# Kernel optimization log

Hardware: AMD Instinct MI355X
Metric: run time of the kernel (lower is better)

Reference implementation:

```python
import jax, jax.numpy as jnp
import numpy as np

N_NODES = 100_000
N_EDGES = 1_600_000
HID = 64
TXT = 384
N_LAYERS = 2
BATCH = 1024


def setup_inputs() -> dict:
    key = jax.random.key(0)
    ks = jax.random.split(key, 13)
    s = 0.05
    return {
        "text_emb": jax.random.normal(ks[0], (N_NODES, TXT), dtype=jnp.float32),
        "weights": jax.random.uniform(ks[1], (N_EDGES,), dtype=jnp.float32),
        "W_enc": jax.random.normal(ks[2], (TXT, HID), dtype=jnp.float32) * s,
        "b_enc": jax.random.normal(ks[3], (HID,), dtype=jnp.float32) * s,
        "Wself_f": jax.random.normal(ks[4], (N_LAYERS, HID, HID), dtype=jnp.float32) * s,
        "Wneigh_f": jax.random.normal(ks[5], (N_LAYERS, HID, HID), dtype=jnp.float32) * s,
        "b_f": jax.random.normal(ks[6], (N_LAYERS, HID), dtype=jnp.float32) * s,
        "Wself_r": jax.random.normal(ks[7], (N_LAYERS, HID, HID), dtype=jnp.float32) * s,
        "Wneigh_r": jax.random.normal(ks[8], (N_LAYERS, HID, HID), dtype=jnp.float32) * s,
        "b_r": jax.random.normal(ks[9], (N_LAYERS, HID), dtype=jnp.float32) * s,
        "src": jax.random.randint(ks[10], (N_EDGES,), 0, N_NODES, dtype=jnp.int32),
        "dst": jax.random.randint(ks[11], (N_EDGES,), 0, N_NODES, dtype=jnp.int32),
        "ids_idx": jax.random.randint(ks[12], (BATCH,), 0, N_NODES, dtype=jnp.int32),
    }


def _inv_degree(idx, n, e_dtype):
    deg = jax.ops.segment_sum(jnp.ones((idx.shape[0],), dtype=e_dtype), idx, num_segments=n)
    return jnp.where(deg > 0, 1.0 / deg, 0.0)  # zero in-degree -> 0 (DGL mean)


def _sage_mean(x, src, dst, w, inv_deg, Wself, Wneigh, b):
    # DGL SAGEConv('mean') with edge_weight: neigh = mean_over_in_edges(w * h_src)
    m = w[:, None] * x[src]                                   # [E, H] gather
    neigh = jax.ops.segment_sum(m, dst, num_segments=x.shape[0]) * inv_deg[:, None]
    return x @ Wself + neigh @ Wneigh + b


def reference(text_emb, weights, W_enc, b_enc, Wself_f, Wneigh_f, b_f,
              Wself_r, Wneigh_r, b_r, src, dst, ids_idx):
    n = text_emb.shape[0]
    inv_f = _inv_degree(dst, n, text_emb.dtype)   # forward graph: aggregate into dst
    inv_r = _inv_degree(src, n, text_emb.dtype)   # reversed graph: aggregate into src
    x = text_emb @ W_enc + b_enc                  # text encoder
    for l in range(Wself_f.shape[0]):
        y = jax.nn.relu(_sage_mean(x, src, dst, weights, inv_f,
                                   Wself_f[l], Wneigh_f[l], b_f[l]))
        y = y + jax.nn.relu(_sage_mean(x, dst, src, weights, inv_r,
                                       Wself_r[l], Wneigh_r[l], b_r[l]))
        x = x + y                                 # skip connection
    feat = x[ids_idx]                             # [B, H]
    return feat / jnp.linalg.norm(feat, axis=1, keepdims=True)
```

## Files before the change

### kernel.cpp

```cpp
#include <hip/hip_runtime.h>

#define NN 100000
#define NE 1600000
#define HID 64
#define TXT 384
#define BATCH 1024
#define NBUCK 391
#define SBLK 256
#define EPB ((NE + SBLK - 1) / SBLK)
#define LDA 40
#define LDK2 72

typedef __attribute__((ext_vector_type(8))) short short8;
typedef __attribute__((ext_vector_type(4))) float float4v;

__device__ __forceinline__ ushort f2bf(float f) {
  unsigned u = __float_as_uint(f);
  unsigned r = (u + 0x7fffu + ((u >> 16) & 1u)) >> 16;
  return (ushort)r;
}
__device__ __forceinline__ float bf2f(ushort u) {
  return __uint_as_float(((unsigned)u) << 16);
}
__device__ __forceinline__ short8 pack8(float4 a, float4 b) {
  short8 s;
  s[0] = (short)f2bf(a.x); s[1] = (short)f2bf(a.y);
  s[2] = (short)f2bf(a.z); s[3] = (short)f2bf(a.w);
  s[4] = (short)f2bf(b.x); s[5] = (short)f2bf(b.y);
  s[6] = (short)f2bf(b.z); s[7] = (short)f2bf(b.w);
  return s;
}

__global__ void k_clear(unsigned char* __restrict__ idmap,
                        unsigned char* __restrict__ flag, int* __restrict__ nf) {
  int i = blockIdx.x * 256 + threadIdx.x;
  if (i < NN) { idmap[i] = 0; flag[i] = 0; }
  if (i == 0) *nf = 0;
}

__global__ void k_seed(const int* __restrict__ ids,
                       unsigned char* __restrict__ idmap,
                       unsigned char* __restrict__ flag) {
  int b = blockIdx.x * 256 + threadIdx.x;
  if (b < BATCH) { int r = ids[b]; idmap[r] = 1; flag[r] = 1; }
}

__global__ void k_fedges(const int* __restrict__ src, const int* __restrict__ dst,
                         const unsigned char* __restrict__ idmap,
                         unsigned char* __restrict__ flag) {
  const int t = threadIdx.x, blk = blockIdx.x;
  const int e0 = blk * EPB, e1 = min(NE, e0 + EPB);
  for (int e = e0 + t; e < e1; e += 256) {
    int s = src[e], d = dst[e];
    if (idmap[d]) flag[s] = 1;
    if (idmap[s]) flag[d] = 1;
  }
}

__global__ void k_compact(const unsigned char* __restrict__ flag,
                          int* __restrict__ frows, int* __restrict__ nf) {
  int i = blockIdx.x * 256 + threadIdx.x;
  if (i < NN && flag[i]) frows[atomicAdd(nf, 1)] = i;
}

__global__ void k_hist2(const int* __restrict__ src, const int* __restrict__ dst,
                        const unsigned char* __restrict__ flag,
                        int* __restrict__ cm_f, int* __restrict__ cm_r) {
  __shared__ int hf[NBUCK], hr[NBUCK];
  const int t = threadIdx.x, blk = blockIdx.x;
  for (int i = t; i < NBUCK; i += 256) { hf[i] = 0; hr[i] = 0; }
  __syncthreads();
  const int e0 = blk * EPB, e1 = min(NE, e0 + EPB);
  for (int e = e0 + t; e < e1; e += 256) {
    int s = src[e], d = dst[e];
    if (flag[d]) atomicAdd(&hf[d >> 8], 1);
    if (flag[s]) atomicAdd(&hr[s >> 8], 1);
  }
  __syncthreads();
  for (int i = t; i < NBUCK; i += 256) {
    cm_f[i * SBLK + blk] = hf[i];
    cm_r[i * SBLK + blk] = hr[i];
  }
}

__global__ void k_scan1(int* __restrict__ cm_f, int* __restrict__ cm_r,
                        int* __restrict__ btot) {
  __shared__ int tmp[256];
  const int t = threadIdx.x;
  int b = blockIdx.x;
  int* cm = (b < NBUCK) ? cm_f : cm_r;
  int bucket = (b < NBUCK) ? b : b - NBUCK;
  int* row = cm + bucket * SBLK;
  int v = row[t];
  tmp[t] = v; __syncthreads();
  for (int d = 1; d < 256; d <<= 1) {
    int s = tmp[t]; if (t >= d) s += tmp[t - d];
    __syncthreads(); tmp[t] = s; __syncthreads();
  }
  row[t] = tmp[t] - v;
  if (t == 255) btot[b] = tmp[t];
}

__global__ void k_scan2(const int* __restrict__ btot,
                        int* __restrict__ bbase_f, int* __restrict__ bbase_r) {
  __shared__ int tmp[512];
  const int t = threadIdx.x;
  int h = (t < NBUCK) ? btot[t] : 0;
  tmp[t] = h; __syncthreads();
  for (int d = 1; d < 512; d <<= 1) {
    int v = tmp[t]; if (t >= d) v += tmp[t - d];
    __syncthreads(); tmp[t] = v; __syncthreads();
  }
  if (t < NBUCK) bbase_f[t] = tmp[t] - h;
  __syncthreads();
  h = (t < NBUCK) ? btot[NBUCK + t] : 0;
  tmp[t] = h; __syncthreads();
  for (int d = 1; d < 512; d <<= 1) {
    int v = tmp[t]; if (t >= d) v += tmp[t - d];
    __syncthreads(); tmp[t] = v; __syncthreads();
  }
  if (t < NBUCK) bbase_r[t] = tmp[t] - h;
}

__global__ void k_scatter2(const int* __restrict__ src, const int* __restrict__ dst,
                           const float* __restrict__ w,
                           const unsigned char* __restrict__ flag,
                           const int* __restrict__ cm_f, const int* __restrict__ cm_r,
                           const int* __restrict__ bbase_f, const int* __restrict__ bbase_r,
                           int2* __restrict__ stg_f, int2* __restrict__ stg_r) {
  __shared__ int cur_f[NBUCK], cur_r[NBUCK];
  const int t = threadIdx.x, blk = blockIdx.x;
  for (int i = t; i < NBUCK; i += 256) {
    cur_f[i] = bbase_f[i] + cm_f[i * SBLK + blk];
    cur_r[i] = bbase_r[i] + cm_r[i * SBLK + blk];
  }
  __syncthreads();
  const int e0 = blk * EPB, e1 = min(NE, e0 + EPB);
  for (int e = e0 + t; e < e1; e += 256) {
    int s = src[e], d = dst[e];
    int wb = __float_as_int(w[e]);
    if (flag[d]) {
      int p = atomicAdd(&cur_f[d >> 8], 1);
      stg_f[p] = make_int2(((d & 255) << 24) | s, wb);
    }
    if (flag[s]) {
      int q = atomicAdd(&cur_r[s >> 8], 1);
      stg_r[q] = make_int2(((s & 255) << 24) | d, wb);
    }
  }
}

__global__ void p_build(const unsigned char* __restrict__ flag,
                        const int2* __restrict__ stgf, const int* __restrict__ btotf,
                        const int* __restrict__ bbasef,
                        int* __restrict__ startf, int* __restrict__ cntf,
                        int2* __restrict__ cvf, int* __restrict__ permf,
                        const int2* __restrict__ stgr, const int* __restrict__ btotr,
                        const int* __restrict__ bbaser,
                        int* __restrict__ startr, int* __restrict__ cntr,
                        int2* __restrict__ cvr, int* __restrict__ permr) {
  int b = blockIdx.x;
  const int2* stg; const int* bcnt; const int* bbase;
  int* start; int* cnt; int2* cv; int* perm;
  if (b < NBUCK) { stg = stgf; bcnt = btotf; bbase = bbasef; start = startf; cnt = cntf; cv = cvf; perm = permf; }
  else { b -= NBUCK; stg = stgr; bcnt = btotr; bbase = bbaser; start = startr; cnt = cntr; cv = cvr; perm = permr; }
  const int base = bbase[b];
  const int n = bcnt[b];
  const int t = threadIdx.x;
  __shared__ int hist[256], tmp[256], cur[256], dh[256], dc[256];
  hist[t] = 0;
  perm[b * 256 + t] = -1;
  __syncthreads();
  for (int i = t; i < n; i += 256) {
    unsigned pk = (unsigned)stg[base + i].x;
    atomicAdd(&hist[pk >> 24], 1);
  }
  __syncthreads();
  const int h = hist[t];
  tmp[t] = h; __syncthreads();
  for (int d = 1; d < 256; d <<= 1) {
    int v = tmp[t]; if (t >= d) v += tmp[t - d];
    __syncthreads(); tmp[t] = v; __syncthreads();
  }
  const int excl = tmp[t] - h;
  const int node = (b << 8) + t;
  const bool valid = (node < NN) && flag[node];
  if (valid) { start[node] = base + excl; cnt[node] = h; }
  cur[t] = excl;
  dh[t] = 0; __syncthreads();
  const int dcap = min(h, 255);
  if (valid) atomicAdd(&dh[dcap], 1);
  __syncthreads();
  int dv = dh[t];
  tmp[t] = dv; __syncthreads();
  for (int d = 1; d < 256; d <<= 1) {
    int v = tmp[t]; if (t >= d) v += tmp[t - d];
    __syncthreads(); tmp[t] = v; __syncthreads();
  }
  dc[t] = tmp[t] - dv;
  __syncthreads();
  if (valid) {
    int pos = atomicAdd(&dc[dcap], 1);
    perm[b * 256 + pos] = node;
  }
  __syncthreads();
  for (int i = t; i < n; i += 256) {
    int2 en = stg[base + i];
    unsigned d8 = ((unsigned)en.x) >> 24;
    int pos = atomicAdd(&cur[d8], 1);
    cv[base + pos] = make_int2(en.x & 0xFFFFFF, en.y);
  }
}

__global__ void k_gather3(const ushort* __restrict__ xb,
                          const int* __restrict__ permf, const int* __restrict__ startf,
                          const int* __restrict__ cntf, const int2* __restrict__ cvf,
                          ushort* __restrict__ nbf,
                          const int* __restrict__ permr, const int* __restrict__ startr,
                          const int* __restrict__ cntr, const int2* __restrict__ cvr,
                          ushort* __restrict__ nbr) {
  const int BPD = (NBUCK * 256) / 16;
  int b = blockIdx.x;
  const int *perm, *start, *cnt; const int2* cv; ushort* outp;
  if (b < BPD) { perm = permf; start = startf; cnt = cntf; cv = cvf; outp = nbf; }
  else { b -= BPD; perm = permr; start = startr; cnt = cntr; cv = cvr; outp = nbr; }
  const int lane = threadIdx.x & 63;
  const int wave = threadIdx.x >> 6;
  const int slot = b * 16 + wave * 4 + (lane >> 4);
  const int fl = (lane & 15) * 4;
  const int row = perm[slot];
  if (row < 0) return;
  const int s = start[row], c = cnt[row];
  const int e = s + c;
  float a0 = 0.f, a1 = 0.f, a2 = 0.f, a3 = 0.f;
  int j = s;
  for (; j + 4 <= e; j += 4) {
    int2 e0 = cv[j], e1 = cv[j + 1], e2 = cv[j + 2], e3 = cv[j + 3];
    uint2 v0 = *(const uint2*)(xb + (size_t)e0.x * 64 + fl);
    uint2 v1 = *(const uint2*)(xb + (size_t)e1.x * 64 + fl);
    uint2 v2 = *(const uint2*)(xb + (size_t)e2.x * 64 + fl);
    uint2 v3 = *(const uint2*)(xb + (size_t)e3.x * 64 + fl);
    float w0 = __int_as_float(e0.y), w1 = __int_as_float(e1.y);
    float w2 = __int_as_float(e2.y), w3 = __int_as_float(e3.y);
    a0 += w0 * bf2f((ushort)v0.x); a1 += w0 * bf2f((ushort)(v0.x >> 16));
    a2 += w0 * bf2f((ushort)v0.y); a3 += w0 * bf2f((ushort)(v0.y >> 16));
    a0 += w1 * bf2f((ushort)v1.x); a1 += w1 * bf2f((ushort)(v1.x >> 16));
    a2 += w1 * bf2f((ushort)v1.y); a3 += w1 * bf2f((ushort)(v1.y >> 16));
    a0 += w2 * bf2f((ushort)v2.x); a1 += w2 * bf2f((ushort)(v2.x >> 16));
    a2 += w2 * bf2f((ushort)v2.y); a3 += w2 * bf2f((ushort)(v2.y >> 16));
    a0 += w3 * bf2f((ushort)v3.x); a1 += w3 * bf2f((ushort)(v3.x >> 16));
    a2 += w3 * bf2f((ushort)v3.y); a3 += w3 * bf2f((ushort)(v3.y >> 16));
  }
  for (; j < e; ++j) {
    int2 ee = cv[j];
    uint2 v = *(const uint2*)(xb + (size_t)ee.x * 64 + fl);
    float ww = __int_as_float(ee.y);
    a0 += ww * bf2f((ushort)v.x); a1 += ww * bf2f((ushort)(v.x >> 16));
    a2 += ww * bf2f((ushort)v.y); a3 += ww * bf2f((ushort)(v.y >> 16));
  }
  float inv = (c > 0) ? 1.0f / (float)c : 0.f;
  uint2 pv;
  pv.x = (uint)f2bf(a0 * inv) | ((uint)f2bf(a1 * inv) << 16);
  pv.y = (uint)f2bf(a2 * inv) | ((uint)f2bf(a3 * inv) << 16);
  *(uint2*)(outp + (size_t)row * 64 + fl) = pv;
}

__global__ void k_bgather(const ushort* __restrict__ xb, const int* __restrict__ ids,
                          const int* __restrict__ startf, const int* __restrict__ cntf,
                          const int2* __restrict__ cvf, ushort* __restrict__ nbf,
                          const int* __restrict__ startr, const int* __restrict__ cntr,
                          const int2* __restrict__ cvr, ushort* __restrict__ nbr) {
  const int lane = threadIdx.x & 63;
  const int wave = threadIdx.x >> 6;
  const int fl = (lane & 15) * 4;
  const int t = blockIdx.x * 16 + wave * 4 + (lane >> 4);
  const int rev = (t >= BATCH);
  const int b = rev ? t - BATCH : t;
  const int row = ids[b];
  const int* start = rev ? startr : startf;
  const int* cnt   = rev ? cntr   : cntf;
  const int2* cv   = rev ? cvr    : cvf;
  ushort* outp     = rev ? nbr    : nbf;
  const int s = start[row], c = cnt[row];
  const int e = s + c;
  float a0 = 0.f, a1 = 0.f, a2 = 0.f, a3 = 0.f;
  int j = s;
  for (; j + 4 <= e; j += 4) {
    int2 e0 = cv[j], e1 = cv[j + 1], e2 = cv[j + 2], e3 = cv[j + 3];
    uint2 v0 = *(const uint2*)(xb + (size_t)e0.x * 64 + fl);
    uint2 v1 = *(const uint2*)(xb + (size_t)e1.x * 64 + fl);
    uint2 v2 = *(const uint2*)(xb + (size_t)e2.x * 64 + fl);
    uint2 v3 = *(const uint2*)(xb + (size_t)e3.x * 64 + fl);
    float w0 = __int_as_float(e0.y), w1 = __int_as_float(e1.y);
    float w2 = __int_as_float(e2.y), w3 = __int_as_float(e3.y);
    a0 += w0 * bf2f((ushort)v0.x); a1 += w0 * bf2f((ushort)(v0.x >> 16));
    a2 += w0 * bf2f((ushort)v0.y); a3 += w0 * bf2f((ushort)(v0.y >> 16));
    a0 += w1 * bf2f((ushort)v1.x); a1 += w1 * bf2f((ushort)(v1.x >> 16));
    a2 += w1 * bf2f((ushort)v1.y); a3 += w1 * bf2f((ushort)(v1.y >> 16));
    a0 += w2 * bf2f((ushort)v2.x); a1 += w2 * bf2f((ushort)(v2.x >> 16));
    a2 += w2 * bf2f((ushort)v2.y); a3 += w2 * bf2f((ushort)(v2.y >> 16));
    a0 += w3 * bf2f((ushort)v3.x); a1 += w3 * bf2f((ushort)(v3.x >> 16));
    a2 += w3 * bf2f((ushort)v3.y); a3 += w3 * bf2f((ushort)(v3.y >> 16));
  }
  for (; j < e; ++j) {
    int2 ee = cv[j];
    uint2 v = *(const uint2*)(xb + (size_t)ee.x * 64 + fl);
    float ww = __int_as_float(ee.y);
    a0 += ww * bf2f((ushort)v.x); a1 += ww * bf2f((ushort)(v.x >> 16));
    a2 += ww * bf2f((ushort)v.y); a3 += ww * bf2f((ushort)(v.y >> 16));
  }
  float inv = (c > 0) ? 1.0f / (float)c : 0.f;
  uint2 pv;
  pv.x = (uint)f2bf(a0 * inv) | ((uint)f2bf(a1 * inv) << 16);
  pv.y = (uint)f2bf(a2 * inv) | ((uint)f2bf(a3 * inv) << 16);
  *(uint2*)(outp + (size_t)b * 64 + fl) = pv;
}

__global__ void k_wtile(const float* __restrict__ W, ushort* __restrict__ Wt) {
  int b = blockIdx.x;
  int ch = b >> 2, nt = b & 3;
  int lane = threadIdx.x;
  int quad = lane >> 4, lr = lane & 15;
  short8 s;
  #pragma unroll
  for (int j = 0; j < 8; ++j)
    s[j] = (short)f2bf(W[(ch * 32 + quad * 8 + j) * 64 + nt * 16 + lr]);
  *(short8*)&Wt[((size_t)b * 64 + lane) * 8] = s;
}

__launch_bounds__(256)
__global__ void k_enc3(const float* __restrict__ T, const ushort* __restrict__ Wt,
                       const float* __restrict__ bias,
                       float* __restrict__ x, ushort* __restrict__ xb) {
  __shared__ short As[2][128 * LDA];
  const int tid = threadIdx.x;
  const int row0 = blockIdx.x * 128;
  const int wave = tid >> 6, lane = tid & 63;
  const int quad = lane >> 4, lr = lane & 15;
  const int srow = tid >> 1, shalf = (tid & 1) * 16;
  const int grow = min(row0 + srow, NN - 1);
  const float* tp = T + (size_t)grow * TXT + shalf;

  float4 pa0 = *(const float4*)(tp);
  float4 pa1 = *(const float4*)(tp + 4);
  float4 pa2 = *(const float4*)(tp + 8);
  float4 pa3 = *(const float4*)(tp + 12);
  *(short8*)&As[0][srow * LDA + shalf] = pack8(pa0, pa1);
  *(short8*)&As[0][srow * LDA + shalf + 8] = pack8(pa2, pa3);
  pa0 = *(const float4*)(tp + 32);
  pa1 = *(const float4*)(tp + 36);
  pa2 = *(const float4*)(tp + 40);
  pa3 = *(const float4*)(tp + 44);
  __syncthreads();

  const ushort* pw = Wt + lane * 8;
  float4v acc[2][4] = {};
  #pragma unroll
  for (int ch = 0; ch < 12; ++ch) {
    const short* Ac = As[ch & 1];
    short8 af0 = *(const short8*)&Ac[(wave * 32 + lr) * LDA + quad * 8];
    short8 af1 = *(const short8*)&Ac[(wave * 32 + 16 + lr) * LDA + quad * 8];
    #pragma unroll
    for (int nt = 0; nt < 4; ++nt) {
      short8 bfrag = *(const short8*)(pw + (size_t)(ch * 4 + nt) * 512);
      acc[0][nt] = __builtin_amdgcn_mfma_f32_16x16x32_bf16(af0, bfrag, acc[0][nt], 0, 0, 0);
      acc[1][nt] = __builtin_amdgcn_mfma_f32_16x16x32_bf16(af1, bfrag, acc[1][nt], 0, 0, 0);
    }
    if (ch < 11) {
      short* An = As[(ch + 1) & 1];
      *(short8*)&An[srow * LDA + shalf] = pack8(pa0, pa1);
      *(short8*)&An[srow * LDA + shalf + 8] = pack8(pa2, pa3);
      if (ch + 2 < 12) {
        const float* q = tp + (ch + 2) * 32;
        pa0 = *(const float4*)(q);
        pa1 = *(const float4*)(q + 4);
        pa2 = *(const float4*)(q + 8);
        pa3 = *(const float4*)(q + 12);
      }
      __syncthreads();
    }
  }
  #pragma unroll
  for (int nt = 0; nt < 4; ++nt) {
    const int col = nt * 16 + lr;
    const float bcol = bias[col];
    #pragma unroll
    for (int mt = 0; mt < 2; ++mt) {
      #pragma unroll
      for (int r = 0; r < 4; ++r) {
        const int row = row0 + wave * 32 + mt * 16 + quad * 4 + r;
        if (row < NN) {
          float v = acc[mt][nt][r] + bcol;
          x[(size_t)row * 64 + col] = v;
          xb[(size_t)row * 64 + col] = f2bf(v);
        }
      }
    }
  }
}

__launch_bounds__(256)
__global__ void k_layerf(const int* __restrict__ frows, const int* __restrict__ nfp,
                         const ushort* __restrict__ xbin,
                         const ushort* __restrict__ nbf, const ushort* __restrict__ nbr,
                         const float* __restrict__ Wsf, const float* __restrict__ Wnf,
                         const float* __restrict__ bfv,
                         const float* __restrict__ Wsr, const float* __restrict__ Wnr,
                         const float* __restrict__ brv,
                         float* __restrict__ x, ushort* __restrict__ xb) {
  const int nfv = *nfp;
  const int row0 = blockIdx.x * 128;
  if (row0 >= nfv) return;
  __shared__ short B4[4 * 64 * LDK2];
  __shared__ short As[128 * LDK2];
  const int tid = threadIdx.x;
  const int wave = tid >> 6, lane = tid & 63;
  const int quad = lane >> 4, lr = lane & 15;

  {
    #pragma unroll
    for (int j = 0; j < 16; ++j) {
      int idx = j * 256 + tid;
      int k = idx >> 6, n = idx & 63;
      B4[0 * 64 * LDK2 + n * LDK2 + k] = (short)f2bf(Wsf[idx]);
      B4[1 * 64 * LDK2 + n * LDK2 + k] = (short)f2bf(Wsr[idx]);
      B4[2 * 64 * LDK2 + n * LDK2 + k] = (short)f2bf(Wnf[idx]);
      B4[3 * 64 * LDK2 + n * LDK2 + k] = (short)f2bf(Wnr[idx]);
    }
  }
  const int srow = tid >> 1, half = (tid & 1) * 32;
  const int slot = row0 + srow;
  const int grow = frows[(slot < nfv) ? slot : 0];
  {
    const uint4* s = (const uint4*)(xbin + (size_t)grow * 64 + half);
    uint4* d = (uint4*)&As[srow * LDK2 + half];
    d[0] = s[0]; d[1] = s[1]; d[2] = s[2]; d[3] = s[3];
  }
  const uint4* pf = (const uint4*)(nbf + (size_t)grow * 64 + half);
  uint4 p0 = pf[0], p1 = pf[1], p2 = pf[2], p3 = pf[3];
  __syncthreads();

  float4v accf[2][4] = {}, accr[2][4] = {};
  #pragma unroll
  for (int kk = 0; kk < 64; kk += 32) {
    short8 a0 = *(const short8*)&As[(wave * 32 + lr) * LDK2 + kk + quad * 8];
    short8 a1 = *(const short8*)&As[(wave * 32 + 16 + lr) * LDK2 + kk + quad * 8];
    #pragma unroll
    for (int nt = 0; nt < 4; ++nt) {
      short8 bs = *(const short8*)&B4[0 * 64 * LDK2 + (nt * 16 + lr) * LDK2 + kk + quad * 8];
      accf[0][nt] = __builtin_amdgcn_mfma_f32_16x16x32_bf16(a0, bs, accf[0][nt], 0, 0, 0);
      accf[1][nt] = __builtin_amdgcn_mfma_f32_16x16x32_bf16(a1, bs, accf[1][nt], 0, 0, 0);
      short8 bq = *(const short8*)&B4[1 * 64 * LDK2 + (nt * 16 + lr) * LDK2 + kk + quad * 8];
      accr[0][nt] = __builtin_amdgcn_mfma_f32_16x16x32_bf16(a0, bq, accr[0][nt], 0, 0, 0);
      accr[1][nt] = __builtin_amdgcn_mfma_f32_16x16x32_bf16(a1, bq, accr[1][nt], 0, 0, 0);
    }
  }
  __syncthreads();
  { uint4* d = (uint4*)&As[srow * LDK2 + half]; d[0] = p0; d[1] = p1; d[2] = p2; d[3] = p3; }
  {
    const uint4* pr = (const uint4*)(nbr + (size_t)grow * 64 + half);
    p0 = pr[0]; p1 = pr[1]; p2 = pr[2]; p3 = pr[3];
  }
  __syncthreads();
  #pragma unroll
  for (int kk = 0; kk < 64; kk += 32) {
    short8 a0 = *(const short8*)&As[(wave * 32 + lr) * LDK2 + kk + quad * 8];
    short8 a1 = *(const short8*)&As[(wave * 32 + 16 + lr) * LDK2 + kk + quad * 8];
    #pragma unroll
    for (int nt = 0; nt < 4; ++nt) {
      short8 bs = *(const short8*)&B4[2 * 64 * LDK2 + (nt * 16 + lr) * LDK2 + kk + quad * 8];
      accf[0][nt] = __builtin_amdgcn_mfma_f32_16x16x32_bf16(a0, bs, accf[0][nt], 0, 0, 0);
      accf[1][nt] = __builtin_amdgcn_mfma_f32_16x16x32_bf16(a1, bs, accf[1][nt], 0, 0, 0);
    }
  }
  __syncthreads();
  { uint4* d = (uint4*)&As[srow * LDK2 + half]; d[0] = p0; d[1] = p1; d[2] = p2; d[3] = p3; }
  __syncthreads();
  #pragma unroll
  for (int kk = 0; kk < 64; kk += 32) {
    short8 a0 = *(const short8*)&As[(wave * 32 + lr) * LDK2 + kk + quad * 8];
    short8 a1 = *(const short8*)&As[(wave * 32 + 16 + lr) * LDK2 + kk + quad * 8];
    #pragma unroll
    for (int nt = 0; nt < 4; ++nt) {
      short8 bs = *(const short8*)&B4[3 * 64 * LDK2 + (nt * 16 + lr) * LDK2 + kk + quad * 8];
      accr[0][nt] = __builtin_amdgcn_mfma_f32_16x16x32_bf16(a0, bs, accr[0][nt], 0, 0, 0);
      accr[1][nt] = __builtin_amdgcn_mfma_f32_16x16x32_bf16(a1, bs, accr[1][nt], 0, 0, 0);
    }
  }
  #pragma unroll
  for (int nt = 0; nt < 4; ++nt) {
    const int col = nt * 16 + lr;
    const float bf_c = bfv[col], br_c = brv[col];
    #pragma unroll
    for (int mt = 0; mt < 2; ++mt) {
      #pragma unroll
      for (int r = 0; r < 4; ++r) {
        const int rl = wave * 32 + mt * 16 + quad * 4 + r;
        const int slotE = row0 + rl;
        if (slotE < nfv) {
          const int node = frows[slotE];
          size_t idx = (size_t)node * 64 + col;
          float v = x[idx] + fmaxf(accf[mt][nt][r] + bf_c, 0.f)
                           + fmaxf(accr[mt][nt][r] + br_c, 0.f);
          x[idx] = v;
          xb[idx] = f2bf(v);
        }
      }
    }
  }
}

__launch_bounds__(256)
__global__ void k_blayer(const ushort* __restrict__ xbin, const float* __restrict__ x,
                         const int* __restrict__ ids,
                         const ushort* __restrict__ nbf, const ushort* __restrict__ nbr,
                         const float* __restrict__ Wsf, const float* __restrict__ Wnf,
                         const float* __restrict__ bfv,
                         const float* __restrict__ Wsr, const float* __restrict__ Wnr,
                         const float* __restrict__ brv,
                         float* __restrict__ out) {
  __shared__ short B4[4 * 64 * LDK2];
  __shared__ short As[128 * LDK2];
  const int tid = threadIdx.x;
  const int b0 = blockIdx.x * 128;
  const int wave = tid >> 6, lane = tid & 63;
  const int quad = lane >> 4, lr = lane & 15;

  #pragma unroll
  for (int j = 0; j < 16; ++j) {
    int idx = j * 256 + tid;
    int k = idx >> 6, n = idx & 63;
    B4[0 * 64 * LDK2 + n * LDK2 + k] = (short)f2bf(Wsf[idx]);
    B4[1 * 64 * LDK2 + n * LDK2 + k] = (short)f2bf(Wsr[idx]);
    B4[2 * 64 * LDK2 + n * LDK2 + k] = (short)f2bf(Wnf[idx]);
    B4[3 * 64 * LDK2 + n * LDK2 + k] = (short)f2bf(Wnr[idx]);
  }
  const int srow = tid >> 1, half = (tid & 1) * 32;
  const int node0 = ids[b0 + srow];
  {
    const uint4* s = (const uint4*)(xbin + (size_t)node0 * 64 + half);
    uint4* d = (uint4*)&As[srow * LDK2 + half];
    d[0] = s[0]; d[1] = s[1]; d[2] = s[2]; d[3] = s[3];
  }
  __syncthreads();

  float4v accf[2][4] = {}, accr[2][4] = {};
  #pragma unroll
  for (int kk = 0; kk < 64; kk += 32) {
    short8 a0 = *(const short8*)&As[(wave * 32 + lr) * LDK2 + kk + quad * 8];
    short8 a1 = *(const short8*)&As[(wave * 32 + 16 + lr) * LDK2 + kk + quad * 8];
    #pragma unroll
    for (int nt = 0; nt < 4; ++nt) {
      short8 bs = *(const short8*)&B4[0 * 64 * LDK2 + (nt * 16 + lr) * LDK2 + kk + quad * 8];
      accf[0][nt] = __builtin_amdgcn_mfma_f32_16x16x32_bf16(a0, bs, accf[0][nt], 0, 0, 0);
      accf[1][nt] = __builtin_amdgcn_mfma_f32_16x16x32_bf16(a1, bs, accf[1][nt], 0, 0, 0);
      short8 bq = *(const short8*)&B4[1 * 64 * LDK2 + (nt * 16 + lr) * LDK2 + kk + quad * 8];
      accr[0][nt] = __builtin_amdgcn_mfma_f32_16x16x32_bf16(a0, bq, accr[0][nt], 0, 0, 0);
      accr[1][nt] = __builtin_amdgcn_mfma_f32_16x16x32_bf16(a1, bq, accr[1][nt], 0, 0, 0);
    }
  }
  __syncthreads();
  {
    const uint4* s = (const uint4*)(nbf + (size_t)(b0 + srow) * 64 + half);
    uint4* d = (uint4*)&As[srow * LDK2 + half];
    d[0] = s[0]; d[1] = s[1]; d[2] = s[2]; d[3] = s[3];
  }
  __syncthreads();
  #pragma unroll
  for (int kk = 0; kk < 64; kk += 32) {
    short8 a0 = *(const short8*)&As[(wave * 32 + lr) * LDK2 + kk + quad * 8];
    short8 a1 = *(const short8*)&As[(wave * 32 + 16 + lr) * LDK2 + kk + quad * 8];
    #pragma unroll
    for (int nt = 0; nt < 4; ++nt) {
      short8 bs = *(const short8*)&B4[2 * 64 * LDK2 + (nt * 16 + lr) * LDK2 + kk + quad * 8];
      accf[0][nt] = __builtin_amdgcn_mfma_f32_16x16x32_bf16(a0, bs, accf[0][nt], 0, 0, 0);
      accf[1][nt] = __builtin_amdgcn_mfma_f32_16x16x32_bf16(a1, bs, accf[1][nt], 0, 0, 0);
    }
  }
  __syncthreads();
  {
    const uint4* s = (const uint4*)(nbr + (size_t)(b0 + srow) * 64 + half);
    uint4* d = (uint4*)&As[srow * LDK2 + half];
    d[0] = s[0]; d[1] = s[1]; d[2] = s[2]; d[3] = s[3];
  }
  __syncthreads();
  #pragma unroll
  for (int kk = 0; kk < 64; kk += 32) {
    short8 a0 = *(const short8*)&As[(wave * 32 + lr) * LDK2 + kk + quad * 8];
    short8 a1 = *(const short8*)&As[(wave * 32 + 16 + lr) * LDK2 + kk + quad * 8];
    #pragma unroll
    for (int nt = 0; nt < 4; ++nt) {
      short8 bs = *(const short8*)&B4[3 * 64 * LDK2 + (nt * 16 + lr) * LDK2 + kk + quad * 8];
      accr[0][nt] = __builtin_amdgcn_mfma_f32_16x16x32_bf16(a0, bs, accr[0][nt], 0, 0, 0);
      accr[1][nt] = __builtin_amdgcn_mfma_f32_16x16x32_bf16(a1, bs, accr[1][nt], 0, 0, 0);
    }
  }
  float vv[2][4][4];
  #pragma unroll
  for (int nt = 0; nt < 4; ++nt) {
    const int col = nt * 16 + lr;
    const float bf_c = bfv[col], br_c = brv[col];
    #pragma unroll
    for (int mt = 0; mt < 2; ++mt) {
      #pragma unroll
      for (int r = 0; r < 4; ++r) {
        const int rl = wave * 32 + mt * 16 + quad * 4 + r;
        const int node = ids[b0 + rl];
        vv[mt][nt][r] = x[(size_t)node * 64 + col]
                      + fmaxf(accf[mt][nt][r] + bf_c, 0.f)
                      + fmaxf(accr[mt][nt][r] + br_c, 0.f);
      }
    }
  }
  #pragma unroll
  for (int mt = 0; mt < 2; ++mt) {
    #pragma unroll
    for (int r = 0; r < 4; ++r) {
      float s = 0.f;
      #pragma unroll
      for (int nt = 0; nt < 4; ++nt) s += vv[mt][nt][r] * vv[mt][nt][r];
      s += __shfl_xor(s, 1); s += __shfl_xor(s, 2);
      s += __shfl_xor(s, 4); s += __shfl_xor(s, 8);
      const int rl = wave * 32 + mt * 16 + quad * 4 + r;
      const float inv = 1.f / sqrtf(s);
      #pragma unroll
      for (int nt = 0; nt < 4; ++nt)
        out[(size_t)(b0 + rl) * 64 + nt * 16 + lr] = vv[mt][nt][r] * inv;
    }
  }
}

extern "C" void kernel_launch(void* const* d_in, const int* in_sizes, int n_in,
                              void* d_out, int out_size, void* d_ws, size_t ws_size,
                              hipStream_t stream) {
  const float* text = (const float*)d_in[0];
  const float* wts  = (const float*)d_in[1];
  const float* Wenc = (const float*)d_in[2];
  const float* benc = (const float*)d_in[3];
  const float* Wsf  = (const float*)d_in[4];
  const float* Wnf  = (const float*)d_in[5];
  const float* bf   = (const float*)d_in[6];
  const float* Wsr  = (const float*)d_in[7];
  const float* Wnr  = (const float*)d_in[8];
  const float* br   = (const float*)d_in[9];
  const int*   src  = (const int*)d_in[10];
  const int*   dst  = (const int*)d_in[11];
  const int*   ids  = (const int*)d_in[12];
  float* out = (float*)d_out;

  char* ws = (char*)d_ws;
  size_t o = 0;
  auto alloc = [&](size_t f32elems) {
    void* p = ws + o;
    o += f32elems * 4;
    o = (o + 255) & ~(size_t)255;
    return p;
  };
  float*  x   = (float*)alloc((size_t)NN * 64);
  ushort* xb  = (ushort*)alloc((size_t)NN * 32);
  ushort* nbf = (ushort*)alloc((size_t)NN * 32);
  ushort* nbr = (ushort*)alloc((size_t)NN * 32);
  ushort* Wt  = (ushort*)alloc(48 * 512 / 2);
  int2*   cvf = (int2*)alloc((size_t)NE * 2);
  int2*   cvr = (int2*)alloc((size_t)NE * 2);
  int* cm_f    = (int*)alloc((size_t)NBUCK * SBLK);
  int* cm_r    = (int*)alloc((size_t)NBUCK * SBLK);
  int* btot    = (int*)alloc(2 * NBUCK);
  int* bbase_f = (int*)alloc(NBUCK);
  int* bbase_r = (int*)alloc(NBUCK);
  int* startf  = (int*)alloc(NN);
  int* cntf    = (int*)alloc(NN);
  int* startr  = (int*)alloc(NN);
  int* cntr    = (int*)alloc(NN);
  int* permf   = (int*)alloc((size_t)NBUCK * 256);
  int* permr   = (int*)alloc((size_t)NBUCK * 256);
  unsigned char* idmap = (unsigned char*)alloc(NN / 4 + 64);
  unsigned char* flag  = (unsigned char*)alloc(NN / 4 + 64);
  int* frows = (int*)alloc(NN);
  int* nf    = (int*)alloc(64);

  int2* stg_f = (int2*)nbf;
  int2* stg_r = (int2*)nbr;

  const int EB2 = (NN + 127) / 128;

  k_wtile<<<48, 64, 0, stream>>>(Wenc, Wt);
  k_clear<<<NBUCK, 256, 0, stream>>>(idmap, flag, nf);
  k_seed<<<(BATCH + 255) / 256, 256, 0, stream>>>(ids, idmap, flag);
  k_fedges<<<SBLK, 256, 0, stream>>>(src, dst, idmap, flag);
  k_hist2<<<SBLK, 256, 0, stream>>>(src, dst, flag, cm_f, cm_r);
  k_scan1<<<2 * NBUCK, 256, 0, stream>>>(cm_f, cm_r, btot);
  k_scan2<<<1, 512, 0, stream>>>(btot, bbase_f, bbase_r);
  k_scatter2<<<SBLK, 256, 0, stream>>>(src, dst, wts, flag, cm_f, cm_r,
                                       bbase_f, bbase_r, stg_f, stg_r);
  p_build<<<2 * NBUCK, 256, 0, stream>>>(flag,
                                         stg_f, btot, bbase_f, startf, cntf, cvf, permf,
                                         stg_r, btot + NBUCK, bbase_r, startr, cntr, cvr, permr);
  k_compact<<<NBUCK, 256, 0, stream>>>(flag, frows, nf);
  k_enc3<<<EB2, 256, 0, stream>>>(text, Wt, benc, x, xb);

  const int GB3 = 2 * ((NBUCK * 256) / 16);
  k_gather3<<<GB3, 256, 0, stream>>>(xb, permf, startf, cntf, cvf, nbf,
                                     permr, startr, cntr, cvr, nbr);
  k_layerf<<<EB2, 256, 0, stream>>>(frows, nf, xb, nbf, nbr,
                                    Wsf, Wnf, bf, Wsr, Wnr, br, x, xb);
  k_bgather<<<(2 * BATCH) / 16, 256, 0, stream>>>(xb, ids, startf, cntf, cvf, nbf,
                                                  startr, cntr, cvr, nbr);
  k_blayer<<<BATCH / 128, 256, 0, stream>>>(xb, x, ids, nbf, nbr,
                                            Wsf + HID * HID, Wnf + HID * HID, bf + HID,
                                            Wsr + HID * HID, Wnr + HID * HID, br + HID,
                                            out);
}
```

Before: 482.3 us.

## Merge encoder GEMM, histogram and compaction into one launch; use wave-shuffle scans

Folds the text-encoder GEMM, the per-block edge histogram and the frontier compaction into one heterogeneous kernel, selected by block index, so these independent stages run concurrently. The weight tiling is merged into the clear kernel. The LDS Hillis-Steele scans are replaced by wave shuffle scans. The encoder now writes fp32 x only for flagged rows, which cuts write traffic. Fewer launches and overlapping independent work are the goals. The cost is that the fused kernel's blocks are unequal in size, and its LDS footprint is fixed by the GEMM branch.

```diff
diff --git a/kernel.cpp b/kernel.cpp
--- a/kernel.cpp
+++ b/kernel.cpp
@@ -10,6 +10,7 @@
 #define EPB ((NE + SBLK - 1) / SBLK)
 #define LDA 40
 #define LDK2 72
+#define EB2 782
 
 typedef __attribute__((ext_vector_type(8))) short short8;
 typedef __attribute__((ext_vector_type(4))) float float4v;
@@ -31,18 +32,49 @@
   return s;
 }
 
-__global__ void k_clear(unsigned char* __restrict__ idmap,
-                        unsigned char* __restrict__ flag, int* __restrict__ nf) {
-  int i = blockIdx.x * 256 + threadIdx.x;
-  if (i < NN) { idmap[i] = 0; flag[i] = 0; }
-  if (i == 0) *nf = 0;
+__device__ __forceinline__ int scan_incl(int v, int* lds8) {
+  const int lane = threadIdx.x & 63, wv = threadIdx.x >> 6;
+  const int nw = blockDim.x >> 6;
+  #pragma unroll
+  for (int d = 1; d < 64; d <<= 1) {
+    int t = __shfl_up(v, d);
+    if (lane >= d) v += t;
+  }
+  if (lane == 63) lds8[wv] = v;
+  __syncthreads();
+  int add = 0;
+  for (int i = 0; i < nw - 1; ++i)
+    if (i < wv) add += lds8[i];
+  __syncthreads();
+  return v + add;
+}
+
+__global__ void k_init(const float* __restrict__ W, ushort* __restrict__ Wt,
+                       unsigned char* __restrict__ idmap,
+                       unsigned char* __restrict__ flag, int* __restrict__ nf) {
+  const int b = blockIdx.x, t = threadIdx.x;
+  if (b < 12) {
+    const int unit = b * 4 + (t >> 6);
+    const int lane = t & 63;
+    const int ch = unit >> 2, nt = unit & 3;
+    const int quad = lane >> 4, lr = lane & 15;
+    short8 s;
+    #pragma unroll
+    for (int j = 0; j < 8; ++j)
+      s[j] = (short)f2bf(W[(ch * 32 + quad * 8 + j) * 64 + nt * 16 + lr]);
+    *(short8*)&Wt[((size_t)unit * 64 + lane) * 8] = s;
+  } else {
+    const int i = (b - 12) * 256 + t;
+    if (i < NN / 4) { ((int*)idmap)[i] = 0; ((int*)flag)[i] = 0; }
+    if (i == 0) *nf = 0;
+  }
 }
 
 __global__ void k_seed(const int* __restrict__ ids,
                        unsigned char* __restrict__ idmap,
                        unsigned char* __restrict__ flag) {
-  int b = blockIdx.x * 256 + threadIdx.x;
-  if (b < BATCH) { int r = ids[b]; idmap[r] = 1; flag[r] = 1; }
+  const int b = threadIdx.x;
+  if (b < BATCH) { const int r = ids[b]; idmap[r] = 1; flag[r] = 1; }
 }
 
 __global__ void k_fedges(const int* __restrict__ src, const int* __restrict__ dst,
@@ -51,75 +83,135 @@
   const int t = threadIdx.x, blk = blockIdx.x;
   const int e0 = blk * EPB, e1 = min(NE, e0 + EPB);
   for (int e = e0 + t; e < e1; e += 256) {
-    int s = src[e], d = dst[e];
+    const int s = src[e], d = dst[e];
     if (idmap[d]) flag[s] = 1;
     if (idmap[s]) flag[d] = 1;
   }
 }
 
-__global__ void k_compact(const unsigned char* __restrict__ flag,
-                          int* __restrict__ frows, int* __restrict__ nf) {
-  int i = blockIdx.x * 256 + threadIdx.x;
-  if (i < NN && flag[i]) frows[atomicAdd(nf, 1)] = i;
-}
-
-__global__ void k_hist2(const int* __restrict__ src, const int* __restrict__ dst,
-                        const unsigned char* __restrict__ flag,
-                        int* __restrict__ cm_f, int* __restrict__ cm_r) {
-  __shared__ int hf[NBUCK], hr[NBUCK];
-  const int t = threadIdx.x, blk = blockIdx.x;
-  for (int i = t; i < NBUCK; i += 256) { hf[i] = 0; hr[i] = 0; }
-  __syncthreads();
-  const int e0 = blk * EPB, e1 = min(NE, e0 + EPB);
-  for (int e = e0 + t; e < e1; e += 256) {
-    int s = src[e], d = dst[e];
-    if (flag[d]) atomicAdd(&hf[d >> 8], 1);
-    if (flag[s]) atomicAdd(&hr[s >> 8], 1);
-  }
-  __syncthreads();
-  for (int i = t; i < NBUCK; i += 256) {
-    cm_f[i * SBLK + blk] = hf[i];
-    cm_r[i * SBLK + blk] = hr[i];
+__launch_bounds__(256)
+__global__ void k_mega(const float* __restrict__ T, const ushort* __restrict__ Wt,
+                       const float* __restrict__ bias,
+                       const unsigned char* __restrict__ flag,
+                       float* __restrict__ x, ushort* __restrict__ xb,
+                       const int* __restrict__ src, const int* __restrict__ dst,
+                       int* __restrict__ cm_f, int* __restrict__ cm_r,
+                       int* __restrict__ frows, int* __restrict__ nf) {
+  __shared__ char sm[2 * 128 * LDA * 2];
+  const int bb = blockIdx.x;
+  const int tid = threadIdx.x;
+  if (bb < EB2) {
+    short (*As)[128 * LDA] = (short (*)[128 * LDA])sm;
+    const int row0 = bb * 128;
+    const int wave = tid >> 6, lane = tid & 63;
+    const int quad = lane >> 4, lr = lane & 15;
+    const int srow = tid >> 1, shalf = (tid & 1) * 16;
+    const int grow = min(row0 + srow, NN - 1);
+    const float* tp = T + (size_t)grow * TXT + shalf;
+
+    float4 pa0 = *(const float4*)(tp);
+    float4 pa1 = *(const float4*)(tp + 4);
+    float4 pa2 = *(const float4*)(tp + 8);
+    float4 pa3 = *(const float4*)(tp + 12);
+    *(short8*)&As[0][srow * LDA + shalf] = pack8(pa0, pa1);
+    *(short8*)&As[0][srow * LDA + shalf + 8] = pack8(pa2, pa3);
+    pa0 = *(const float4*)(tp + 32);
+    pa1 = *(const float4*)(tp + 36);
+    pa2 = *(const float4*)(tp + 40);
+    pa3 = *(const float4*)(tp + 44);
+    __syncthreads();
+
+    const ushort* pw = Wt + lane * 8;
+    float4v acc[2][4] = {};
+    #pragma unroll
+    for (int ch = 0; ch < 12; ++ch) {
+      const short* Ac = As[ch & 1];
+      short8 af0 = *(const short8*)&Ac[(wave * 32 + lr) * LDA + quad * 8];
+      short8 af1 = *(const short8*)&Ac[(wave * 32 + 16 + lr) * LDA + quad * 8];
+      #pragma unroll
+      for (int nt = 0; nt < 4; ++nt) {
+        short8 bfrag = *(const short8*)(pw + (size_t)(ch * 4 + nt) * 512);
+        acc[0][nt] = __builtin_amdgcn_mfma_f32_16x16x32_bf16(af0, bfrag, acc[0][nt], 0, 0, 0);
+        acc[1][nt] = __builtin_amdgcn_mfma_f32_16x16x32_bf16(af1, bfrag, acc[1][nt], 0, 0, 0);
+      }
+      if (ch < 11) {
+        short* An = As[(ch + 1) & 1];
+        *(short8*)&An[srow * LDA + shalf] = pack8(pa0, pa1);
+        *(short8*)&An[srow * LDA + shalf + 8] = pack8(pa2, pa3);
+        if (ch + 2 < 12) {
+          const float* q = tp + (ch + 2) * 32;
+          pa0 = *(const float4*)(q);
+          pa1 = *(const float4*)(q + 4);
+          pa2 = *(const float4*)(q + 8);
+          pa3 = *(const float4*)(q + 12);
+        }
+        __syncthreads();
+      }
+    }
+    #pragma unroll
+    for (int nt = 0; nt < 4; ++nt) {
+      const int col = nt * 16 + lr;
+      const float bcol = bias[col];
+      #pragma unroll
+      for (int mt = 0; mt < 2; ++mt) {
+        #pragma unroll
+        for (int r = 0; r < 4; ++r) {
+          const int row = row0 + wave * 32 + mt * 16 + quad * 4 + r;
+          if (row < NN) {
+            const float v = acc[mt][nt][r] + bcol;
+            const size_t idx = (size_t)row * 64 + col;
+            xb[idx] = f2bf(v);
+            if (flag[row]) x[idx] = v;
+          }
+        }
+      }
+    }
+  } else if (bb < EB2 + SBLK) {
+    int* hf = (int*)sm; int* hr = hf + NBUCK;
+    const int blk = bb - EB2;
+    for (int i = tid; i < NBUCK; i += 256) { hf[i] = 0; hr[i] = 0; }
+    __syncthreads();
+    const int e0 = blk * EPB, e1 = min(NE, e0 + EPB);
+    for (int e = e0 + tid; e < e1; e += 256) {
+      const int s = src[e], d = dst[e];
+      if (flag[d]) atomicAdd(&hf[d >> 8], 1);
+      if (flag[s]) atomicAdd(&hr[s >> 8], 1);
+    }
+    __syncthreads();
+    for (int i = tid; i < NBUCK; i += 256) {
+      cm_f[i * SBLK + blk] = hf[i];
+      cm_r[i * SBLK + blk] = hr[i];
+    }
+  } else {
+    const int i = (bb - EB2 - SBLK) * 256 + tid;
+    if (i < NN && flag[i]) frows[atomicAdd(nf, 1)] = i;
   }
 }
 
 __global__ void k_scan1(int* __restrict__ cm_f, int* __restrict__ cm_r,
                         int* __restrict__ btot) {
-  __shared__ int tmp[256];
+  __shared__ int lds8[8];
   const int t = threadIdx.x;
-  int b = blockIdx.x;
+  const int b = blockIdx.x;
   int* cm = (b < NBUCK) ? cm_f : cm_r;
-  int bucket = (b < NBUCK) ? b : b - NBUCK;
+  const int bucket = (b < NBUCK) ? b : b - NBUCK;
   int* row = cm + bucket * SBLK;
-  int v = row[t];
-  tmp[t] = v; __syncthreads();
-  for (int d = 1; d < 256; d <<= 1) {
-    int s = tmp[t]; if (t >= d) s += tmp[t - d];
-    __syncthreads(); tmp[t] = s; __syncthreads();
-  }
-  row[t] = tmp[t] - v;
-  if (t == 255) btot[b] = tmp[t];
+  const int v = row[t];
+  const int incl = scan_incl(v, lds8);
+  row[t] = incl - v;
+  if (t == 255) btot[b] = incl;
 }
 
 __global__ void k_scan2(const int* __restrict__ btot,
                         int* __restrict__ bbase_f, int* __restrict__ bbase_r) {
-  __shared__ int tmp[512];
+  __shared__ int lds8[8];
   const int t = threadIdx.x;
   int h = (t < NBUCK) ? btot[t] : 0;
-  tmp[t] = h; __syncthreads();
-  for (int d = 1; d < 512; d <<= 1) {
-    int v = tmp[t]; if (t >= d) v += tmp[t - d];
-    __syncthreads(); tmp[t] = v; __syncthreads();
-  }
-  if (t < NBUCK) bbase_f[t] = tmp[t] - h;
-  __syncthreads();
+  int incl = scan_incl(h, lds8);
+  if (t < NBUCK) bbase_f[t] = incl - h;
   h = (t < NBUCK) ? btot[NBUCK + t] : 0;
-  tmp[t] = h; __syncthreads();
-  for (int d = 1; d < 512; d <<= 1) {
-    int v = tmp[t]; if (t >= d) v += tmp[t - d];
-    __syncthreads(); tmp[t] = v; __syncthreads();
-  }
-  if (t < NBUCK) bbase_r[t] = tmp[t] - h;
+  incl = scan_incl(h, lds8);
+  if (t < NBUCK) bbase_r[t] = incl - h;
 }
 
 __global__ void k_scatter2(const int* __restrict__ src, const int* __restrict__ dst,
@@ -137,14 +229,14 @@
   __syncthreads();
   const int e0 = blk * EPB, e1 = min(NE, e0 + EPB);
   for (int e = e0 + t; e < e1; e += 256) {
-    int s = src[e], d = dst[e];
-    int wb = __float_as_int(w[e]);
+    const int s = src[e], d = dst[e];
+    const int wb = __float_as_int(w[e]);
     if (flag[d]) {
-      int p = atomicAdd(&cur_f[d >> 8], 1);
+      const int p = atomicAdd(&cur_f[d >> 8], 1);
       stg_f[p] = make_int2(((d & 255) << 24) | s, wb);
     }
     if (flag[s]) {
-      int q = atomicAdd(&cur_r[s >> 8], 1);
+      const int q = atomicAdd(&cur_r[s >> 8], 1);
       stg_r[q] = make_int2(((s & 255) << 24) | d, wb);
     }
   }
@@ -167,22 +259,17 @@
   const int base = bbase[b];
   const int n = bcnt[b];
   const int t = threadIdx.x;
-  __shared__ int hist[256], tmp[256], cur[256], dh[256], dc[256];
+  __shared__ int hist[256], cur[256], dh[256], dc[256], lds8[8];
   hist[t] = 0;
   perm[b * 256 + t] = -1;
   __syncthreads();
   for (int i = t; i < n; i += 256) {
-    unsigned pk = (unsigned)stg[base + i].x;
+    const unsigned pk = (unsigned)stg[base + i].x;
     atomicAdd(&hist[pk >> 24], 1);
   }
   __syncthreads();
   const int h = hist[t];
-  tmp[t] = h; __syncthreads();
-  for (int d = 1; d < 256; d <<= 1) {
-    int v = tmp[t]; if (t >= d) v += tmp[t - d];
-    __syncthreads(); tmp[t] = v; __syncthreads();
-  }
-  const int excl = tmp[t] - h;
+  const int excl = scan_incl(h, lds8) - h;
   const int node = (b << 8) + t;
   const bool valid = (node < NN) && flag[node];
   if (valid) { start[node] = base + excl; cnt[node] = h; }
@@ -191,23 +278,18 @@
   const int dcap = min(h, 255);
   if (valid) atomicAdd(&dh[dcap], 1);
   __syncthreads();
-  int dv = dh[t];
-  tmp[t] = dv; __syncthreads();
-  for (int d = 1; d < 256; d <<= 1) {
-    int v = tmp[t]; if (t >= d) v += tmp[t - d];
-    __syncthreads(); tmp[t] = v; __syncthreads();
-  }
-  dc[t] = tmp[t] - dv;
+  const int dv = dh[t];
+  dc[t] = scan_incl(dv, lds8) - dv;
   __syncthreads();
   if (valid) {
-    int pos = atomicAdd(&dc[dcap], 1);
+    const int pos = atomicAdd(&dc[dcap], 1);
     perm[b * 256 + pos] = node;
   }
   __syncthreads();
   for (int i = t; i < n; i += 256) {
-    int2 en = stg[base + i];
-    unsigned d8 = ((unsigned)en.x) >> 24;
-    int pos = atomicAdd(&cur[d8], 1);
+    const int2 en = stg[base + i];
+    const unsigned d8 = ((unsigned)en.x) >> 24;
+    const int pos = atomicAdd(&cur[d8], 1);
     cv[base + pos] = make_int2(en.x & 0xFFFFFF, en.y);
   }
 }
@@ -258,7 +340,7 @@
     a0 += ww * bf2f((ushort)v.x); a1 += ww * bf2f((ushort)(v.x >> 16));
     a2 += ww * bf2f((ushort)v.y); a3 += ww * bf2f((ushort)(v.y >> 16));
   }
-  float inv = (c > 0) ? 1.0f / (float)c : 0.f;
+  const float inv = (c > 0) ? 1.0f / (float)c : 0.f;
   uint2 pv;
   pv.x = (uint)f2bf(a0 * inv) | ((uint)f2bf(a1 * inv) << 16);
   pv.y = (uint)f2bf(a2 * inv) | ((uint)f2bf(a3 * inv) << 16);
@@ -309,94 +391,11 @@
     a0 += ww * bf2f((ushort)v.x); a1 += ww * bf2f((ushort)(v.x >> 16));
     a2 += ww * bf2f((ushort)v.y); a3 += ww * bf2f((ushort)(v.y >> 16));
   }
-  float inv = (c > 0) ? 1.0f / (float)c : 0.f;
+  const float inv = (c > 0) ? 1.0f / (float)c : 0.f;
   uint2 pv;
   pv.x = (uint)f2bf(a0 * inv) | ((uint)f2bf(a1 * inv) << 16);
   pv.y = (uint)f2bf(a2 * inv) | ((uint)f2bf(a3 * inv) << 16);
   *(uint2*)(outp + (size_t)b * 64 + fl) = pv;
-}
-
-__global__ void k_wtile(const float* __restrict__ W, ushort* __restrict__ Wt) {
-  int b = blockIdx.x;
-  int ch = b >> 2, nt = b & 3;
-  int lane = threadIdx.x;
-  int quad = lane >> 4, lr = lane & 15;
-  short8 s;
-  #pragma unroll
-  for (int j = 0; j < 8; ++j)
-    s[j] = (short)f2bf(W[(ch * 32 + quad * 8 + j) * 64 + nt * 16 + lr]);
-  *(short8*)&Wt[((size_t)b * 64 + lane) * 8] = s;
-}
-
-__launch_bounds__(256)
-__global__ void k_enc3(const float* __restrict__ T, const ushort* __restrict__ Wt,
-                       const float* __restrict__ bias,
-                       float* __restrict__ x, ushort* __restrict__ xb) {
-  __shared__ short As[2][128 * LDA];
-  const int tid = threadIdx.x;
-  const int row0 = blockIdx.x * 128;
-  const int wave = tid >> 6, lane = tid & 63;
-  const int quad = lane >> 4, lr = lane & 15;
-  const int srow = tid >> 1, shalf = (tid & 1) * 16;
-  const int grow = min(row0 + srow, NN - 1);
-  const float* tp = T + (size_t)grow * TXT + shalf;
-
-  float4 pa0 = *(const float4*)(tp);
-  float4 pa1 = *(const float4*)(tp + 4);
-  float4 pa2 = *(const float4*)(tp + 8);
-  float4 pa3 = *(const float4*)(tp + 12);
-  *(short8*)&As[0][srow * LDA + shalf] = pack8(pa0, pa1);
-  *(short8*)&As[0][srow * LDA + shalf + 8] = pack8(pa2, pa3);
-  pa0 = *(const float4*)(tp + 32);
-  pa1 = *(const float4*)(tp + 36);
-  pa2 = *(const float4*)(tp + 40);
-  pa3 = *(const float4*)(tp + 44);
-  __syncthreads();
-
-  const ushort* pw = Wt + lane * 8;
-  float4v acc[2][4] = {};
-  #pragma unroll
-  for (int ch = 0; ch < 12; ++ch) {
-    const short* Ac = As[ch & 1];
-    short8 af0 = *(const short8*)&Ac[(wave * 32 + lr) * LDA + quad * 8];
-    short8 af1 = *(const short8*)&Ac[(wave * 32 + 16 + lr) * LDA + quad * 8];
-    #pragma unroll
-    for (int nt = 0; nt < 4; ++nt) {
-      short8 bfrag = *(const short8*)(pw + (size_t)(ch * 4 + nt) * 512);
-      acc[0][nt] = __builtin_amdgcn_mfma_f32_16x16x32_bf16(af0, bfrag, acc[0][nt], 0, 0, 0);
-      acc[1][nt] = __builtin_amdgcn_mfma_f32_16x16x32_bf16(af1, bfrag, acc[1][nt], 0, 0, 0);
-    }
-    if (ch < 11) {
-      short* An = As[(ch + 1) & 1];
-      *(short8*)&An[srow * LDA + shalf] = pack8(pa0, pa1);
-      *(short8*)&An[srow * LDA + shalf + 8] = pack8(pa2, pa3);
-      if (ch + 2 < 12) {
-        const float* q = tp + (ch + 2) * 32;
-        pa0 = *(const float4*)(q);
-        pa1 = *(const float4*)(q + 4);
-        pa2 = *(const float4*)(q + 8);
-        pa3 = *(const float4*)(q + 12);
-      }
-      __syncthreads();
-    }
-  }
-  #pragma unroll
-  for (int nt = 0; nt < 4; ++nt) {
-    const int col = nt * 16 + lr;
-    const float bcol = bias[col];
-    #pragma unroll
-    for (int mt = 0; mt < 2; ++mt) {
-      #pragma unroll
-      for (int r = 0; r < 4; ++r) {
-        const int row = row0 + wave * 32 + mt * 16 + quad * 4 + r;
-        if (row < NN) {
-          float v = acc[mt][nt][r] + bcol;
-          x[(size_t)row * 64 + col] = v;
-          xb[(size_t)row * 64 + col] = f2bf(v);
-        }
-      }
-    }
-  }
 }
 
 __launch_bounds__(256)
@@ -499,9 +498,9 @@
         const int slotE = row0 + rl;
         if (slotE < nfv) {
           const int node = frows[slotE];
-          size_t idx = (size_t)node * 64 + col;
-          float v = x[idx] + fmaxf(accf[mt][nt][r] + bf_c, 0.f)
-                           + fmaxf(accr[mt][nt][r] + br_c, 0.f);
+          const size_t idx = (size_t)node * 64 + col;
+          const float v = x[idx] + fmaxf(accf[mt][nt][r] + bf_c, 0.f)
+                                 + fmaxf(accr[mt][nt][r] + br_c, 0.f);
           x[idx] = v;
           xb[idx] = f2bf(v);
         }
@@ -682,13 +681,11 @@
   int2* stg_f = (int2*)nbf;
   int2* stg_r = (int2*)nbr;
 
-  const int EB2 = (NN + 127) / 128;
-
-  k_wtile<<<48, 64, 0, stream>>>(Wenc, Wt);
-  k_clear<<<NBUCK, 256, 0, stream>>>(idmap, flag, nf);
-  k_seed<<<(BATCH + 255) / 256, 256, 0, stream>>>(ids, idmap, flag);
+  k_init<<<12 + 98, 256, 0, stream>>>(Wenc, Wt, idmap, flag, nf);
+  k_seed<<<1, 1024, 0, stream>>>(ids, idmap, flag);
   k_fedges<<<SBLK, 256, 0, stream>>>(src, dst, idmap, flag);
-  k_hist2<<<SBLK, 256, 0, stream>>>(src, dst, flag, cm_f, cm_r);
+  k_mega<<<EB2 + SBLK + 391, 256, 0, stream>>>(text, Wt, benc, flag, x, xb,
+                                               src, dst, cm_f, cm_r, frows, nf);
   k_scan1<<<2 * NBUCK, 256, 0, stream>>>(cm_f, cm_r, btot);
   k_scan2<<<1, 512, 0, stream>>>(btot, bbase_f, bbase_r);
   k_scatter2<<<SBLK, 256, 0, stream>>>(src, dst, wts, flag, cm_f, cm_r,
@@ -696,9 +693,6 @@
   p_build<<<2 * NBUCK, 256, 0, stream>>>(flag,
                                          stg_f, btot, bbase_f, startf, cntf, cvf, permf,
                                          stg_r, btot + NBUCK, bbase_r, startr, cntr, cvr, permr);
-  k_compact<<<NBUCK, 256, 0, stream>>>(flag, frows, nf);
-  k_enc3<<<EB2, 256, 0, stream>>>(text, Wt, benc, x, xb);
-
   const int GB3 = 2 * ((NBUCK * 256) / 16);
   k_gather3<<<GB3, 256, 0, stream>>>(xb, permf, startf, cntf, cvf, nbf,
                                      permr, startr, cntr, cvr, nbr);
```

After: 457.3 us. 1.05x faster.
